# Optimization experiments

Hardware: AMD Instinct MI355X
Metric: run time of the kernel (lower is better)

Reference implementation:

```python
import jax, jax.numpy as jnp
import numpy as np

B, S, H = 2, 1024, 1024
NH, HD = 8, 128
E, TOPK, MI = 8, 2, 1024
SI = 2 * MI  # shared experts intermediate (n_shared_experts=2)
EPS = 1e-6
THETA = 10000.0


def setup_inputs() -> dict:
    key = jax.random.key(0)
    ks = jax.random.split(key, 16)
    w = lambda k, shp: (0.02 * jax.random.normal(k, shp, dtype=jnp.float32))
    # RoPE tables [S, HD]
    inv_freq = 1.0 / (THETA ** (np.arange(0, HD, 2, dtype=np.float32) / HD))
    t = np.arange(S, dtype=np.float32)
    freqs = np.outer(t, inv_freq)
    emb = np.concatenate([freqs, freqs], axis=-1)
    return {
        "hidden_states": jax.random.normal(ks[0], (B, S, H), dtype=jnp.float32),
        "ln1_w": jnp.ones((H,), jnp.float32),
        "ln2_w": jnp.ones((H,), jnp.float32),
        "q_w": w(ks[1], (H, H)),
        "k_w": w(ks[2], (H, H)),
        "v_w": w(ks[3], (H, H)),
        "o_w": w(ks[4], (H, H)),
        "cos": jnp.asarray(np.cos(emb), jnp.float32),
        "sin": jnp.asarray(np.sin(emb), jnp.float32),
        "gate_w": w(ks[5], (E, H)),
        "eg_w": w(ks[6], (E, MI, H)),
        "eu_w": w(ks[7], (E, MI, H)),
        "ed_w": w(ks[8], (E, H, MI)),
        "sg_w": w(ks[9], (SI, H)),
        "su_w": w(ks[10], (SI, H)),
        "sd_w": w(ks[11], (H, SI)),
    }


def _rmsnorm(x, w):
    return x * jax.lax.rsqrt(jnp.mean(x * x, axis=-1, keepdims=True) + EPS) * w


def _rotate_half(x):
    x1, x2 = jnp.split(x, 2, axis=-1)
    return jnp.concatenate([-x2, x1], axis=-1)


def _attention(x, q_w, k_w, v_w, o_w, cos, sin):
    b, s, h = x.shape
    q = (x @ q_w.T).reshape(b, s, NH, HD)
    k = (x @ k_w.T).reshape(b, s, NH, HD)
    v = (x @ v_w.T).reshape(b, s, NH, HD)
    c = cos[None, :s, None, :]
    sn = sin[None, :s, None, :]
    q = q * c + _rotate_half(q) * sn
    k = k * c + _rotate_half(k) * sn
    scores = jnp.einsum("bqhd,bkhd->bhqk", q, k) / jnp.sqrt(jnp.float32(HD))
    causal = jnp.tril(jnp.ones((s, s), dtype=bool))
    scores = jnp.where(causal[None, None], scores, -jnp.inf)
    p = jax.nn.softmax(scores, axis=-1)
    out = jnp.einsum("bhqk,bkhd->bqhd", p, v).reshape(b, s, h)
    return out @ o_w.T


def _mlp(x, gw, uw, dw):
    return (jax.nn.silu(x @ gw.T) * (x @ uw.T)) @ dw.T


def _moe(x, gate_w, eg_w, eu_w, ed_w, sg_w, su_w, sd_w):
    b, s, h = x.shape
    xt = x.reshape(-1, h)                              # [T, H]
    T = xt.shape[0]
    probs = jax.nn.softmax(xt @ gate_w.T, axis=-1)     # [T, E]
    rw, idx = jax.lax.top_k(probs, TOPK)               # [T, K]
    rw = rw / (jnp.sum(rw, axis=-1, keepdims=True) + 1e-20)  # norm_topk_prob
    # dense combine weights [T, E] (zero for unselected experts)
    w_full = jnp.zeros((T, E), xt.dtype).at[jnp.arange(T)[:, None], idx].add(rw)
    # dense all-expert compute, masked-combined (faithful to per-token loop math)
    g = jax.nn.silu(jnp.einsum("th,eih->tei", xt, eg_w))
    u = jnp.einsum("th,eih->tei", xt, eu_w)
    y = jnp.einsum("tei,ehi->teh", g * u, ed_w)        # [T, E, H]
    routed = jnp.einsum("teh,te->th", y, w_full)
    shared = _mlp(xt, sg_w, su_w, sd_w)
    return (routed + shared).reshape(b, s, h)


def reference(hidden_states, ln1_w, ln2_w, q_w, k_w, v_w, o_w, cos, sin,
              gate_w, eg_w, eu_w, ed_w, sg_w, su_w, sd_w):
    x = hidden_states
    x = x + _attention(_rmsnorm(x, ln1_w), q_w, k_w, v_w, o_w, cos, sin)
    x = x + _moe(_rmsnorm(x, ln2_w), gate_w, eg_w, eu_w, ed_w, sg_w, su_w, sd_w)
    return x
```

## Files before the change

### kernel.cpp

```cpp
#include <hip/hip_runtime.h>

#define B_   2
#define S_   1024
#define H_   1024
#define NH_  8
#define HD_  128
#define E_   8
#define MI_  1024
#define SI_  2048
#define T_   2048
#define CAP_ 2048

typedef unsigned short u16;
typedef __attribute__((ext_vector_type(4))) float f32x4;
typedef __attribute__((ext_vector_type(4))) unsigned short u16x4;
typedef __attribute__((ext_vector_type(8))) __bf16 bf16x8;

__device__ __forceinline__ u16 f2bf(float f) {
  unsigned int u = __builtin_bit_cast(unsigned int, f);
  u = (u + 0x7fffu + ((u >> 16) & 1u)) >> 16;
  return (u16)u;
}
__device__ __forceinline__ float bf2f(u16 u) {
  return __builtin_bit_cast(float, (unsigned int)u << 16);
}
__device__ __forceinline__ float wave_sum(float v) {
#pragma unroll
  for (int o = 32; o; o >>= 1) v += __shfl_down(v, o, 64);
  return v;
}
__device__ __forceinline__ void gll16(const u16* g, u16* l) {
  __builtin_amdgcn_global_load_lds((const __attribute__((address_space(1))) void*)g,
                                   (__attribute__((address_space(3))) void*)l, 16, 0, 0);
}

__global__ void cvt_all(const float* __restrict__ q_w, const float* __restrict__ k_w,
                        const float* __restrict__ v_w, const float* __restrict__ o_w,
                        const float* __restrict__ eg_w, const float* __restrict__ eu_w,
                        const float* __restrict__ ed_w, const float* __restrict__ sg_w,
                        const float* __restrict__ su_w, const float* __restrict__ sd_w,
                        u16* __restrict__ qwb, u16* __restrict__ egu, u16* __restrict__ edb,
                        u16* __restrict__ sgu, u16* __restrict__ sdb) {
  int bid = blockIdx.x, tid = threadIdx.x;
  const float* in;
  u16* outp;
  long f;
  if (bid < 4096) {
    f = ((long)bid * 256 + tid) * 4;
    int seg = (int)(f >> 20);
    in = (seg == 0) ? q_w : (seg == 1) ? k_w : (seg == 2) ? v_w : o_w;
    f32x4 v = *(const f32x4*)(in + (f & 1048575));
    u16x4 r;
#pragma unroll
    for (int c = 0; c < 4; c++) r[c] = f2bf(v[c]);
    *(u16x4*)(qwb + f) = r;
    return;
  } else if (bid < 20480) {
    int rel = bid - 4096;
    int zu = rel >= 8192;
    in = zu ? eu_w : eg_w;
    f = ((long)(rel & 8191) * 256 + tid) * 4;
    long e = f >> 20;
    long rem = f & 1048575;
    long i = rem >> 10, hh = rem & 1023;
    long orow = (i >> 4) * 32 + (i & 15) + (zu ? 16 : 0);
    outp = egu + (e * 2048 + orow) * 1024 + hh;
  } else if (bid < 28672) {
    f = ((long)(bid - 20480) * 256 + tid) * 4;
    in = ed_w;
    outp = edb + f;
  } else if (bid < 32768) {
    int rel = bid - 28672;
    int zu = rel >= 2048;
    in = zu ? su_w : sg_w;
    f = ((long)(rel & 2047) * 256 + tid) * 4;
    long i = f >> 10, hh = f & 1023;
    long orow = (i >> 4) * 32 + (i & 15) + (zu ? 16 : 0);
    outp = sgu + orow * 1024 + hh;
  } else {
    f = ((long)(bid - 32768) * 256 + tid) * 4;
    in = sd_w;
    outp = sdb + f;
  }
  f32x4 v = *(const f32x4*)(in + f);
  u16x4 r;
#pragma unroll
  for (int c = 0; c < 4; c++) r[c] = f2bf(v[c]);
  *(u16x4*)outp = r;
}

__global__ void rmsnorm_cvt(const float* __restrict__ x, const float* __restrict__ w,
                            u16* __restrict__ out) {
  int t = blockIdx.x, tid = threadIdx.x;
  f32x4 v = ((const f32x4*)(x + (long)t * H_))[tid];
  float ss = v[0]*v[0] + v[1]*v[1] + v[2]*v[2] + v[3]*v[3];
  __shared__ float red[4];
  float s = wave_sum(ss);
  if ((tid & 63) == 0) red[tid >> 6] = s;
  __syncthreads();
  float r = rsqrtf((red[0] + red[1] + red[2] + red[3]) * (1.0f / H_) + 1e-6f);
  f32x4 wv = ((const f32x4*)w)[tid];
  u16x4 o;
#pragma unroll
  for (int c = 0; c < 4; c++) o[c] = f2bf(v[c] * r * wv[c]);
  ((u16x4*)(out + (long)t * H_))[tid] = o;
}

__global__ void rmsnorm2_gate(const float* __restrict__ x1, const float* __restrict__ ln2w,
                              const float* __restrict__ gw, u16* __restrict__ xn,
                              int* __restrict__ eidx, float* __restrict__ aw) {
  int t = blockIdx.x, tid = threadIdx.x;
  int lane = tid & 63, wave = tid >> 6;
  f32x4 v = ((const f32x4*)(x1 + (long)t * H_))[tid];
  float ss = v[0]*v[0] + v[1]*v[1] + v[2]*v[2] + v[3]*v[3];
  __shared__ float redS[4];
  __shared__ float redE[4][E_];
  float s = wave_sum(ss);
  if (lane == 0) redS[wave] = s;
  __syncthreads();
  float r = rsqrtf((redS[0] + redS[1] + redS[2] + redS[3]) * (1.0f / H_) + 1e-6f);
  f32x4 wv = ((const f32x4*)ln2w)[tid];
  float xv[4];
  u16x4 o;
#pragma unroll
  for (int c = 0; c < 4; c++) { xv[c] = v[c] * r * wv[c]; o[c] = f2bf(xv[c]); }
  ((u16x4*)(xn + (long)t * H_))[tid] = o;
  float acc[E_];
#pragma unroll
  for (int e = 0; e < E_; e++) {
    f32x4 g = ((const f32x4*)(gw + (long)e * H_))[tid];
    acc[e] = xv[0]*g[0] + xv[1]*g[1] + xv[2]*g[2] + xv[3]*g[3];
  }
#pragma unroll
  for (int e = 0; e < E_; e++) acc[e] = wave_sum(acc[e]);
  if (lane == 0)
#pragma unroll
    for (int e = 0; e < E_; e++) redE[wave][e] = acc[e];
  __syncthreads();
  if (tid == 0) {
    float l[E_];
#pragma unroll
    for (int e = 0; e < E_; e++) l[e] = redE[0][e] + redE[1][e] + redE[2][e] + redE[3][e];
    float mx = l[0];
#pragma unroll
    for (int e = 1; e < E_; e++) mx = fmaxf(mx, l[e]);
    float p[E_], z = 0.f;
#pragma unroll
    for (int e = 0; e < E_; e++) { p[e] = __expf(l[e] - mx); z += p[e]; }
    int e0 = 0;
#pragma unroll
    for (int e = 1; e < E_; e++) if (p[e] > p[e0]) e0 = e;
    int e1 = (e0 == 0) ? 1 : 0;
#pragma unroll
    for (int e = 0; e < E_; e++) if (e != e0 && p[e] > p[e1]) e1 = e;
    float q0 = p[e0] / z, q1 = p[e1] / z;
    float invs = 1.0f / (q0 + q1 + 1e-20f);
    eidx[t * 2] = e0;
    eidx[t * 2 + 1] = e1;
    aw[t * 2] = q0 * invs;
    aw[t * 2 + 1] = q1 * invs;
  }
}

__global__ __launch_bounds__(256) void route_scan(const int* __restrict__ eidx,
                                                  int* __restrict__ arow,
                                                  int* __restrict__ cursor) {
  __shared__ int sc[E_][256];
  int tid = threadIdx.x;
  unsigned c0 = 0, c1 = 0;
  int ebuf[16];
#pragma unroll
  for (int i = 0; i < 16; i++) {
    int e = eidx[tid * 16 + i];
    ebuf[i] = e;
    if (e < 4) c0 += 1u << (8 * e); else c1 += 1u << (8 * (e - 4));
  }
#pragma unroll
  for (int e = 0; e < E_; e++)
    sc[e][tid] = (e < 4) ? (int)((c0 >> (8 * e)) & 0xff) : (int)((c1 >> (8 * (e - 4))) & 0xff);
  __syncthreads();
  for (int st = 1; st < 256; st <<= 1) {
    int v[E_];
#pragma unroll
    for (int e = 0; e < E_; e++) v[e] = (tid >= st) ? sc[e][tid - st] : 0;
    __syncthreads();
#pragma unroll
    for (int e = 0; e < E_; e++) sc[e][tid] += v[e];
    __syncthreads();
  }
  if (tid == 255)
#pragma unroll
    for (int e = 0; e < E_; e++) cursor[e] = sc[e][255];
  int base[E_];
#pragma unroll
  for (int e = 0; e < E_; e++) {
    int own = (e < 4) ? (int)((c0 >> (8 * e)) & 0xff) : (int)((c1 >> (8 * (e - 4))) & 0xff);
    base[e] = sc[e][tid] - own;
  }
  __syncthreads();
#pragma unroll
  for (int e = 0; e < E_; e++) sc[e][tid] = base[e];
  __syncthreads();
  unsigned r0 = 0, r1 = 0;
#pragma unroll
  for (int i = 0; i < 16; i++) {
    int e = ebuf[i];
    int run = (e < 4) ? (int)((r0 >> (8 * e)) & 0xff) : (int)((r1 >> (8 * (e - 4))) & 0xff);
    arow[tid * 16 + i] = e * CAP_ + sc[e][tid] + run;
    if (e < 4) r0 += 1u << (8 * e); else r1 += 1u << (8 * (e - 4));
  }
}

__global__ void rope_cvt(const float* __restrict__ qf, const float* __restrict__ cs,
                         const float* __restrict__ sn, u16* __restrict__ qbb) {
  const float* q = qf + (long)blockIdx.z * 2097152;
  u16* qb = qbb + (long)blockIdx.z * 2097152;
  int rid = blockIdx.x * 2 + (threadIdx.x >> 7);
  int d = threadIdx.x & 127;
  int h = rid & (NH_ - 1);
  int bs = rid >> 3;
  int s = bs & (S_ - 1);
  int b = bs >> 10;
  long base = (long)rid * HD_;
  float v = q[base + d];
  float o = (d < 64) ? (-q[base + d + 64]) : q[base + d - 64];
  float res = v * cs[s * HD_ + d] + o * sn[s * HD_ + d];
  qb[((long)((b * NH_ + h) * S_ + s)) * HD_ + d] = f2bf(res);
}

__global__ void vtrans(const float* __restrict__ v, u16* __restrict__ vt) {
  int bh = blockIdx.z, b = bh >> 3, h = bh & 7;
  int s0 = blockIdx.x * 32, d0 = blockIdx.y * 32;
  __shared__ u16 tile[32][33];
  for (int i = threadIdx.y; i < 32; i += 8) {
    float val = v[(((long)(b * S_ + s0 + i)) * NH_ + h) * HD_ + d0 + threadIdx.x];
    tile[i][threadIdx.x] = f2bf(val);
  }
  __syncthreads();
  for (int i = threadIdx.y; i < 32; i += 8) {
    vt[((long)bh * HD_ + d0 + i) * S_ + s0 + threadIdx.x] = tile[threadIdx.x][i];
  }
}

__global__ __launch_bounds__(256) void flash_part(
    const u16* __restrict__ qb, const u16* __restrict__ kb,
    const u16* __restrict__ vt, u16* __restrict__ Po,
    float* __restrict__ Pm, float* __restrict__ Pl) {
  int item = blockIdx.x;
  int bh = blockIdx.y;
  int qt, ch;
  if (item < 4)       { qt = item;                    ch = 0; }
  else if (item < 12) { qt = 4 + ((item - 4) >> 1);   ch = (item - 4) & 1; }
  else if (item < 24) { qt = 8 + (item - 12) / 3;     ch = (item - 12) % 3; }
  else                { qt = 12 + ((item - 24) >> 2); ch = (item - 24) & 3; }
  int j0 = ch * 4, j1 = min(j0 + 4, qt + 1);

  int tid = threadIdx.x;
  int wavei = tid >> 6, lane = tid & 63;
  int la = lane & 15, qd = lane >> 4;

  __shared__ __align__(16) u16 Ks[64 * 128];
  __shared__ __align__(16) u16 Vs[128 * 64];
  __shared__ __align__(16) u16 Ps[4][16 * 64];

  bf16x8 qf[4];
  const u16* qrow = qb + ((long)bh * S_ + qt * 64 + wavei * 16 + la) * HD_;
#pragma unroll
  for (int ks = 0; ks < 4; ks++)
    qf[ks] = *(const bf16x8*)(qrow + ks * 32 + qd * 8);

  f32x4 oacc[8];
#pragma unroll
  for (int nf = 0; nf < 8; nf++) oacc[nf] = (f32x4){0.f, 0.f, 0.f, 0.f};
  float m_i[4], l_i[4];
#pragma unroll
  for (int r = 0; r < 4; r++) { m_i[r] = -1e30f; l_i[r] = 0.f; }

  const u16* Kbase = kb + (long)bh * S_ * HD_;
  const u16* Vbase = vt + (long)bh * HD_ * S_;
  const float scale = 0.08838834764831845f;
  u16* pw = (u16*)Ps[wavei];
  int swz = la & 7;

  for (int j = j0; j < j1; j++) {
    __syncthreads();
#pragma unroll
    for (int t = 0; t < 4; t++) {
      int blk = t * 4 + wavei;
      int kr = blk * 4 + (lane >> 4);
      int kc = (lane & 15) ^ (kr & 7);
      gll16(Kbase + ((long)j * 64 + kr) * 128 + kc * 8, Ks + blk * 512);
      int vr = blk * 8 + (lane >> 3);
      int vc = (lane & 7) ^ (vr & 7);
      gll16(Vbase + (long)vr * 1024 + j * 64 + vc * 8, Vs + blk * 512);
    }
    __syncthreads();

    f32x4 sacc[4];
#pragma unroll
    for (int jf = 0; jf < 4; jf++) sacc[jf] = (f32x4){0.f, 0.f, 0.f, 0.f};
#pragma unroll
    for (int ks = 0; ks < 4; ks++)
#pragma unroll
      for (int jf = 0; jf < 4; jf++) {
        bf16x8 kfrag = *(const bf16x8*)(Ks + (jf * 16 + la) * 128 + ((ks * 4 + qd) ^ swz) * 8);
        sacc[jf] = __builtin_amdgcn_mfma_f32_16x16x32_bf16(qf[ks], kfrag, sacc[jf], 0, 0, 0);
      }

    float sv[4][4];
    int qglob = qt * 64 + wavei * 16 + qd * 4;
#pragma unroll
    for (int jf = 0; jf < 4; jf++) {
      int kglob = j * 64 + jf * 16 + la;
#pragma unroll
      for (int r = 0; r < 4; r++)
        sv[jf][r] = (kglob <= qglob + r) ? sacc[jf][r] * scale : -1e30f;
    }
    float mnew[4], alpha[4];
#pragma unroll
    for (int r = 0; r < 4; r++) {
      float mx = fmaxf(fmaxf(sv[0][r], sv[1][r]), fmaxf(sv[2][r], sv[3][r]));
#pragma unroll
      for (int o = 1; o < 16; o <<= 1) mx = fmaxf(mx, __shfl_xor(mx, o, 64));
      mnew[r] = fmaxf(m_i[r], mx);
      alpha[r] = __expf(m_i[r] - mnew[r]);
      m_i[r] = mnew[r];
    }
#pragma unroll
    for (int r = 0; r < 4; r++) {
      float sum = 0.f;
#pragma unroll
      for (int jf = 0; jf < 4; jf++) {
        float p = __expf(sv[jf][r] - mnew[r]);
        sv[jf][r] = p;
        sum += p;
      }
#pragma unroll
      for (int o = 1; o < 16; o <<= 1) sum += __shfl_xor(sum, o, 64);
      l_i[r] = l_i[r] * alpha[r] + sum;
    }
#pragma unroll
    for (int jf = 0; jf < 4; jf++)
#pragma unroll
      for (int r = 0; r < 4; r++) {
        int rp = qd * 4 + r;
        int e = jf * 16 + la;
        pw[rp * 64 + (((e >> 3) ^ (rp & 7)) << 3) + (e & 7)] = f2bf(sv[jf][r]);
      }
#pragma unroll
    for (int nf = 0; nf < 8; nf++)
#pragma unroll
      for (int r = 0; r < 4; r++) oacc[nf][r] *= alpha[r];
#pragma unroll
    for (int ks = 0; ks < 2; ks++) {
      bf16x8 pfrag = *(const bf16x8*)(pw + la * 64 + ((ks * 4 + qd) ^ swz) * 8);
#pragma unroll
      for (int nf = 0; nf < 8; nf++) {
        bf16x8 vfrag = *(const bf16x8*)(Vs + (nf * 16 + la) * 64 + (((ks * 4 + qd) & 7) ^ swz) * 8);
        oacc[nf] = __builtin_amdgcn_mfma_f32_16x16x32_bf16(pfrag, vfrag, oacc[nf], 0, 0, 0);
      }
    }
  }

  int pidx = (bh * 16 + qt) * 4 + ch;
  int rowb = wavei * 16 + qd * 4;
  u16* pob = Po + ((long)pidx * 64 + rowb) * 128;
#pragma unroll
  for (int r = 0; r < 4; r++)
#pragma unroll
    for (int nf = 0; nf < 8; nf++)
      pob[(long)r * 128 + nf * 16 + la] = f2bf(oacc[nf][r]);
  if (la == 0)
#pragma unroll
    for (int r = 0; r < 4; r++) {
      Pm[pidx * 64 + rowb + r] = m_i[r];
      Pl[pidx * 64 + rowb + r] = l_i[r];
    }
}

__global__ __launch_bounds__(256) void attn_merge(
    const u16* __restrict__ Po, const float* __restrict__ Pm,
    const float* __restrict__ Pl, u16* __restrict__ attn) {
  int qt = blockIdx.x, bh = blockIdx.y;
  int b = bh >> 3, h = bh & 7;
  int nch = (qt >> 2) + 1;
  int t = threadIdx.x;
  int row = t >> 2, cg = (t & 3) * 32;
  long base = (long)(bh * 16 + qt) * 4;
  float mv[4], wv[4];
  float M = -1e30f;
  for (int c = 0; c < nch; c++) { mv[c] = Pm[(base + c) * 64 + row]; M = fmaxf(M, mv[c]); }
  float L = 0.f;
  for (int c = 0; c < nch; c++) { wv[c] = __expf(mv[c] - M); L += wv[c] * Pl[(base + c) * 64 + row]; }
  float inv = 1.0f / L;
  f32x4 o[8];
#pragma unroll
  for (int k = 0; k < 8; k++) o[k] = (f32x4){0.f, 0.f, 0.f, 0.f};
  for (int c = 0; c < nch; c++) {
    const u16x4* src = (const u16x4*)(Po + ((base + c) * 64 + row) * 128 + cg);
#pragma unroll
    for (int k = 0; k < 8; k++) {
      u16x4 sv = src[k];
#pragma unroll
      for (int e = 0; e < 4; e++) o[k][e] += bf2f(sv[e]) * wv[c];
    }
  }
  u16* dst = attn + ((long)b * S_ + qt * 64 + row) * H_ + h * HD_ + cg;
#pragma unroll
  for (int k = 0; k < 8; k++) {
    u16x4 ov;
#pragma unroll
    for (int c = 0; c < 4; c++) ov[c] = f2bf(o[k][c] * inv);
    ((u16x4*)dst)[k] = ov;
  }
}

__global__ void gather_rows(const u16* __restrict__ xn, const int* __restrict__ arow,
                            u16* __restrict__ xg) {
  int a = blockIdx.x;
  int t = a >> 1;
  int row = arow[a];
  u16x4 v = ((const u16x4*)(xn + (long)t * H_))[threadIdx.x];
  ((u16x4*)(xg + (long)row * H_))[threadIdx.x] = v;
}

__global__ void final_combine(const float* __restrict__ x1, const float* __restrict__ ys,
                              const u16* __restrict__ y, const int* __restrict__ arow,
                              const float* __restrict__ aw, float* __restrict__ out) {
  int t = blockIdx.x;
  int i = threadIdx.x * 4;
  int r0 = arow[t * 2], r1 = arow[t * 2 + 1];
  float w0 = aw[t * 2], w1 = aw[t * 2 + 1];
  f32x4 a = *(const f32x4*)(x1 + (long)t * H_ + i);
  f32x4 b = *(const f32x4*)(ys + (long)t * H_ + i);
  u16x4 y0 = *(const u16x4*)(y + (long)r0 * H_ + i);
  u16x4 y1 = *(const u16x4*)(y + (long)r1 * H_ + i);
  f32x4 o;
#pragma unroll
  for (int c = 0; c < 4; c++)
    o[c] = a[c] + b[c] + w0 * bf2f(y0[c]) + w1 * bf2f(y1[c]);
  *(f32x4*)(out + (long)t * H_ + i) = o;
}

template <int MT, int STORE_BF16, int ADD_RES, int FUSE_SILU>
__global__ __launch_bounds__(256) void gemm_bt(
    const u16* __restrict__ Ag, const u16* __restrict__ Bg, void* __restrict__ Cg,
    const float* __restrict__ Res, int K, int lda, int ldb, int ldc,
    long sAz, long sBz, long sCz, const int* __restrict__ mlimit) {
  constexpr int MR = MT / 32;
  int z = blockIdx.z;
  int m0 = blockIdx.y * MT, n0 = blockIdx.x * 128;
  if (mlimit && m0 >= mlimit[z]) return;
  const u16* A = Ag + z * sAz;
  const u16* B = Bg + z * sBz;
  long cbase = (long)z * sCz;

  __shared__ __align__(16) u16 As[MT * 64];
  __shared__ __align__(16) u16 Bs[128 * 64];
  int tid = threadIdx.x;
  int lane = tid & 63, wave = tid >> 6;
  int wm = (wave & 1) * (MT / 2), wn = (wave >> 1) * 64;
  int la = lane & 15, qd = lane >> 4;
  int sr = lane >> 3;
  int scs = (lane & 7) ^ (sr & 7);

  const u16* ap[MT / 32];
  const u16* bp[4];
#pragma unroll
  for (int t = 0; t < MT / 32; t++)
    ap[t] = A + (long)(m0 + t * 32 + wave * 8 + sr) * lda + scs * 8;
#pragma unroll
  for (int t = 0; t < 4; t++)
    bp[t] = B + (long)(n0 + t * 32 + wave * 8 + sr) * ldb + scs * 8;

  f32x4 acc[MR][4];
#pragma unroll
  for (int i = 0; i < MR; i++)
#pragma unroll
    for (int j = 0; j < 4; j++) acc[i][j] = (f32x4){0.f, 0.f, 0.f, 0.f};

  int sw = la & 7;
  for (int k0 = 0; k0 < K; k0 += 64) {
    __syncthreads();
#pragma unroll
    for (int t = 0; t < MT / 32; t++)
      gll16(ap[t] + k0, As + (t * 32 + wave * 8) * 64);
#pragma unroll
    for (int t = 0; t < 4; t++)
      gll16(bp[t] + k0, Bs + (t * 32 + wave * 8) * 64);
    __syncthreads();
#pragma unroll
    for (int kk = 0; kk < 2; kk++) {
      bf16x8 af[MR], bf[4];
#pragma unroll
      for (int i = 0; i < MR; i++)
        af[i] = *(const bf16x8*)(As + (wm + i * 16 + la) * 64 + (((kk * 4 + qd) ^ sw) << 3));
#pragma unroll
      for (int j = 0; j < 4; j++)
        bf[j] = *(const bf16x8*)(Bs + (wn + j * 16 + la) * 64 + (((kk * 4 + qd) ^ sw) << 3));
#pragma unroll
      for (int i = 0; i < MR; i++)
#pragma unroll
        for (int j = 0; j < 4; j++)
          acc[i][j] = __builtin_amdgcn_mfma_f32_16x16x32_bf16(af[i], bf[j], acc[i][j], 0, 0, 0);
    }
  }

  if (FUSE_SILU) {
#pragma unroll
    for (int i = 0; i < MR; i++) {
#pragma unroll
      for (int jp = 0; jp < 2; jp++) {
        int hcol = ((n0 + wn) >> 1) + (jp << 4) + la;
#pragma unroll
        for (int r = 0; r < 4; r++) {
          int row = m0 + wm + i * 16 + qd * 4 + r;
          float g = acc[i][jp * 2][r], u = acc[i][jp * 2 + 1][r];
          float sg = g / (1.f + __expf(-g));
          ((u16*)Cg)[cbase + (long)row * ldc + hcol] = f2bf(sg * u);
        }
      }
    }
  } else {
#pragma unroll
    for (int i = 0; i < MR; i++) {
#pragma unroll
      for (int j = 0; j < 4; j++) {
        int col = n0 + wn + j * 16 + la;
#pragma unroll
        for (int r = 0; r < 4; r++) {
          int row = m0 + wm + i * 16 + qd * 4 + r;
          float v = acc[i][j][r];
          long ci = cbase + (long)row * ldc + col;
          if (ADD_RES) v += Res[(long)row * ldc + col];
          if (STORE_BF16) ((u16*)Cg)[ci] = f2bf(v);
          else ((float*)Cg)[ci] = v;
        }
      }
    }
  }
}

extern "C" void kernel_launch(void* const* d_in, const int* in_sizes, int n_in,
                              void* d_out, int out_size, void* d_ws, size_t ws_size,
                              hipStream_t stream) {
  const float* hidden = (const float*)d_in[0];
  const float* ln1w = (const float*)d_in[1];
  const float* ln2w = (const float*)d_in[2];
  const float* q_w = (const float*)d_in[3];
  const float* k_w = (const float*)d_in[4];
  const float* v_w = (const float*)d_in[5];
  const float* o_w = (const float*)d_in[6];
  const float* cosp = (const float*)d_in[7];
  const float* sinp = (const float*)d_in[8];
  const float* gate_w = (const float*)d_in[9];
  const float* eg_w = (const float*)d_in[10];
  const float* eu_w = (const float*)d_in[11];
  const float* ed_w = (const float*)d_in[12];
  const float* sg_w = (const float*)d_in[13];
  const float* su_w = (const float*)d_in[14];
  const float* sd_w = (const float*)d_in[15];
  float* out = (float*)d_out;

  char* w = (char*)d_ws;
  const size_t MB = 1u << 20;
  u16* qwb = (u16*)(w + 0 * MB);
  u16* egu = (u16*)(w + 8 * MB);
  u16* edb = (u16*)(w + 40 * MB);
  u16* sgu = (u16*)(w + 56 * MB);
  u16* sdb = (u16*)(w + 64 * MB);
  float* x1 = (float*)(w + 68 * MB);
  u16* xn = (u16*)(w + 76 * MB);
  u16* attn = (u16*)(w + 80 * MB);
  int* cursor = (int*)(w + 84 * MB);
  int* arow = (int*)(w + 84 * MB + 1024);
  float* aw = (float*)(w + 84 * MB + 20 * 1024);
  int* eidx = (int*)(w + 84 * MB + 40 * 1024);
  float* qf = (float*)(w + 85 * MB);
  float* kf = (float*)(w + 93 * MB);
  float* vf = (float*)(w + 101 * MB);
  u16* qb = (u16*)(w + 109 * MB);
  u16* kb = (u16*)(w + 113 * MB);
  u16* vt = (u16*)(w + 117 * MB);
  u16* Po = (u16*)(w + 121 * MB);
  float* Pm = (float*)(w + 155 * MB);
  float* Pl = (float*)(w + 156 * MB);
  u16* xg = (u16*)(w + 85 * MB);
  u16* hbuf = (u16*)(w + 121 * MB);
  u16* y = (u16*)(w + 157 * MB);
  u16* hs = (u16*)(w + 189 * MB);
  float* ys = (float*)(w + 197 * MB);

  const long M1 = 1048576, M2 = 2097152;

  cvt_all<<<34816, 256, 0, stream>>>(q_w, k_w, v_w, o_w, eg_w, eu_w, ed_w,
                                     sg_w, su_w, sd_w, qwb, egu, edb, sgu, sdb);

  rmsnorm_cvt<<<T_, 256, 0, stream>>>(hidden, ln1w, xn);
  gemm_bt<128, 0, 0, 0><<<dim3(8, 16, 3), 256, 0, stream>>>(
      xn, qwb, qf, nullptr, 1024, 1024, 1024, 1024, 0, M1, M2, nullptr);
  rope_cvt<<<dim3(8192, 1, 2), 256, 0, stream>>>(qf, cosp, sinp, qb);
  vtrans<<<dim3(32, 4, 16), dim3(32, 8), 0, stream>>>(vf, vt);
  flash_part<<<dim3(40, 16), 256, 0, stream>>>(qb, kb, vt, Po, Pm, Pl);
  attn_merge<<<dim3(16, 16), 256, 0, stream>>>(Po, Pm, Pl, attn);
  gemm_bt<64, 0, 1, 0><<<dim3(8, 32, 1), 256, 0, stream>>>(
      attn, qwb + 3 * M1, x1, hidden, 1024, 1024, 1024, 1024, 0, 0, 0, nullptr);

  rmsnorm2_gate<<<T_, 256, 0, stream>>>(x1, ln2w, gate_w, xn, eidx, aw);
  route_scan<<<1, 256, 0, stream>>>(eidx, arow, cursor);
  gather_rows<<<4096, 256, 0, stream>>>(xn, arow, xg);
  gemm_bt<128, 1, 0, 1><<<dim3(16, 16, 8), 256, 0, stream>>>(
      xg, egu, hbuf, nullptr, 1024, 1024, 1024, MI_,
      (long)CAP_ * H_, (long)2 * MI_ * H_, (long)CAP_ * MI_, cursor);
  gemm_bt<128, 1, 0, 0><<<dim3(8, 16, 8), 256, 0, stream>>>(
      hbuf, edb, y, nullptr, 1024, 1024, 1024, 1024,
      (long)CAP_ * MI_, (long)H_ * MI_, (long)CAP_ * H_, cursor);
  gemm_bt<128, 1, 0, 1><<<dim3(32, 16, 1), 256, 0, stream>>>(
      xn, sgu, hs, nullptr, 1024, 1024, 1024, SI_, 0, 0, 0, nullptr);
  gemm_bt<64, 0, 0, 0><<<dim3(8, 32, 1), 256, 0, stream>>>(
      hs, sdb, ys, nullptr, 2048, 2048, 2048, 1024, 0, 0, 0, nullptr);

  final_combine<<<T_, 256, 0, stream>>>(x1, ys, y, arow, aw, out);
}
```

Measured before the change: 427.4 us.

## Widen weight conversion, store QKV in bf16, and fuse MoE gather into GEMM

The weight conversion kernel now has each thread handle 16 elements with 8-wide bf16 stores, which cuts the block count by a factor of four. The QKV GEMM writes bf16 instead of fp32, so rope and the V transpose read half the bytes. The MoE gather kernel is removed: route_scan writes a row-to-token index table and the expert up/gate GEMM loads A rows indirectly through it, so the gathered copy is never materialised. This costs a memset and an extra index load per A row, and rounding Q/K to bf16 before RoPE adds a little precision loss.

```diff
diff --git a/kernel.cpp b/kernel.cpp
--- a/kernel.cpp
+++ b/kernel.cpp
@@ -14,6 +14,7 @@
 typedef unsigned short u16;
 typedef __attribute__((ext_vector_type(4))) float f32x4;
 typedef __attribute__((ext_vector_type(4))) unsigned short u16x4;
+typedef __attribute__((ext_vector_type(8))) unsigned short u16x8;
 typedef __attribute__((ext_vector_type(8))) __bf16 bf16x8;
 
 __device__ __forceinline__ u16 f2bf(float f) {
@@ -42,51 +43,53 @@
                         u16* __restrict__ qwb, u16* __restrict__ egu, u16* __restrict__ edb,
                         u16* __restrict__ sgu, u16* __restrict__ sdb) {
   int bid = blockIdx.x, tid = threadIdx.x;
-  const float* in;
-  u16* outp;
-  long f;
-  if (bid < 4096) {
-    f = ((long)bid * 256 + tid) * 4;
+  const float* src;
+  u16* dst;
+  if (bid < 1024) {
+    long f = (long)bid * 4096 + tid * 16;
     int seg = (int)(f >> 20);
-    in = (seg == 0) ? q_w : (seg == 1) ? k_w : (seg == 2) ? v_w : o_w;
-    f32x4 v = *(const f32x4*)(in + (f & 1048575));
-    u16x4 r;
-#pragma unroll
-    for (int c = 0; c < 4; c++) r[c] = f2bf(v[c]);
-    *(u16x4*)(qwb + f) = r;
-    return;
-  } else if (bid < 20480) {
-    int rel = bid - 4096;
-    int zu = rel >= 8192;
-    in = zu ? eu_w : eg_w;
-    f = ((long)(rel & 8191) * 256 + tid) * 4;
-    long e = f >> 20;
-    long rem = f & 1048575;
+    const float* in = (seg == 0) ? q_w : (seg == 1) ? k_w : (seg == 2) ? v_w : o_w;
+    src = in + (f & 1048575);
+    dst = qwb + f;
+  } else if (bid < 5120) {
+    int rel = bid - 1024;
+    int zu = rel >= 2048;
+    long fl = (long)(rel & 2047) * 4096 + tid * 16;
+    long e = fl >> 20;
+    long rem = fl & 1048575;
     long i = rem >> 10, hh = rem & 1023;
     long orow = (i >> 4) * 32 + (i & 15) + (zu ? 16 : 0);
-    outp = egu + (e * 2048 + orow) * 1024 + hh;
-  } else if (bid < 28672) {
-    f = ((long)(bid - 20480) * 256 + tid) * 4;
-    in = ed_w;
-    outp = edb + f;
-  } else if (bid < 32768) {
-    int rel = bid - 28672;
-    int zu = rel >= 2048;
-    in = zu ? su_w : sg_w;
-    f = ((long)(rel & 2047) * 256 + tid) * 4;
-    long i = f >> 10, hh = f & 1023;
+    src = (zu ? eu_w : eg_w) + fl;
+    dst = egu + (e * 2048 + orow) * 1024 + hh;
+  } else if (bid < 7168) {
+    long fl = (long)(bid - 5120) * 4096 + tid * 16;
+    src = ed_w + fl;
+    dst = edb + fl;
+  } else if (bid < 8192) {
+    int rel = bid - 7168;
+    int zu = rel >= 512;
+    long fl = (long)(rel & 511) * 4096 + tid * 16;
+    long i = fl >> 10, hh = fl & 1023;
     long orow = (i >> 4) * 32 + (i & 15) + (zu ? 16 : 0);
-    outp = sgu + orow * 1024 + hh;
+    src = (zu ? su_w : sg_w) + fl;
+    dst = sgu + orow * 1024 + hh;
   } else {
-    f = ((long)(bid - 32768) * 256 + tid) * 4;
-    in = sd_w;
-    outp = sdb + f;
-  }
-  f32x4 v = *(const f32x4*)(in + f);
-  u16x4 r;
-#pragma unroll
-  for (int c = 0; c < 4; c++) r[c] = f2bf(v[c]);
-  *(u16x4*)outp = r;
+    long fl = (long)(bid - 8192) * 4096 + tid * 16;
+    src = sd_w + fl;
+    dst = sdb + fl;
+  }
+  f32x4 v0 = ((const f32x4*)src)[0];
+  f32x4 v1 = ((const f32x4*)src)[1];
+  f32x4 v2 = ((const f32x4*)src)[2];
+  f32x4 v3 = ((const f32x4*)src)[3];
+  u16x8 r0, r1;
+#pragma unroll
+  for (int c = 0; c < 4; c++) {
+    r0[c] = f2bf(v0[c]); r0[c + 4] = f2bf(v1[c]);
+    r1[c] = f2bf(v2[c]); r1[c + 4] = f2bf(v3[c]);
+  }
+  ((u16x8*)dst)[0] = r0;
+  ((u16x8*)dst)[1] = r1;
 }
 
 __global__ void rmsnorm_cvt(const float* __restrict__ x, const float* __restrict__ w,
@@ -164,7 +167,8 @@
 
 __global__ __launch_bounds__(256) void route_scan(const int* __restrict__ eidx,
                                                   int* __restrict__ arow,
-                                                  int* __restrict__ cursor) {
+                                                  int* __restrict__ cursor,
+                                                  int* __restrict__ itok) {
   __shared__ int sc[E_][256];
   int tid = threadIdx.x;
   unsigned c0 = 0, c1 = 0;
@@ -206,14 +210,16 @@
   for (int i = 0; i < 16; i++) {
     int e = ebuf[i];
     int run = (e < 4) ? (int)((r0 >> (8 * e)) & 0xff) : (int)((r1 >> (8 * (e - 4))) & 0xff);
-    arow[tid * 16 + i] = e * CAP_ + sc[e][tid] + run;
+    int row = e * CAP_ + sc[e][tid] + run;
+    arow[tid * 16 + i] = row;
+    itok[row] = (tid * 16 + i) >> 1;
     if (e < 4) r0 += 1u << (8 * e); else r1 += 1u << (8 * (e - 4));
   }
 }
 
-__global__ void rope_cvt(const float* __restrict__ qf, const float* __restrict__ cs,
+__global__ void rope_cvt(const u16* __restrict__ qf, const float* __restrict__ cs,
                          const float* __restrict__ sn, u16* __restrict__ qbb) {
-  const float* q = qf + (long)blockIdx.z * 2097152;
+  const u16* q = qf + (long)blockIdx.z * 2097152;
   u16* qb = qbb + (long)blockIdx.z * 2097152;
   int rid = blockIdx.x * 2 + (threadIdx.x >> 7);
   int d = threadIdx.x & 127;
@@ -222,19 +228,18 @@
   int s = bs & (S_ - 1);
   int b = bs >> 10;
   long base = (long)rid * HD_;
-  float v = q[base + d];
-  float o = (d < 64) ? (-q[base + d + 64]) : q[base + d - 64];
+  float v = bf2f(q[base + d]);
+  float o = (d < 64) ? (-bf2f(q[base + d + 64])) : bf2f(q[base + d - 64]);
   float res = v * cs[s * HD_ + d] + o * sn[s * HD_ + d];
   qb[((long)((b * NH_ + h) * S_ + s)) * HD_ + d] = f2bf(res);
 }
 
-__global__ void vtrans(const float* __restrict__ v, u16* __restrict__ vt) {
+__global__ void vtrans(const u16* __restrict__ v, u16* __restrict__ vt) {
   int bh = blockIdx.z, b = bh >> 3, h = bh & 7;
   int s0 = blockIdx.x * 32, d0 = blockIdx.y * 32;
   __shared__ u16 tile[32][33];
   for (int i = threadIdx.y; i < 32; i += 8) {
-    float val = v[(((long)(b * S_ + s0 + i)) * NH_ + h) * HD_ + d0 + threadIdx.x];
-    tile[i][threadIdx.x] = f2bf(val);
+    tile[i][threadIdx.x] = v[(((long)(b * S_ + s0 + i)) * NH_ + h) * HD_ + d0 + threadIdx.x];
   }
   __syncthreads();
   for (int i = threadIdx.y; i < 32; i += 8) {
@@ -415,15 +420,6 @@
   }
 }
 
-__global__ void gather_rows(const u16* __restrict__ xn, const int* __restrict__ arow,
-                            u16* __restrict__ xg) {
-  int a = blockIdx.x;
-  int t = a >> 1;
-  int row = arow[a];
-  u16x4 v = ((const u16x4*)(xn + (long)t * H_))[threadIdx.x];
-  ((u16x4*)(xg + (long)row * H_))[threadIdx.x] = v;
-}
-
 __global__ void final_combine(const float* __restrict__ x1, const float* __restrict__ ys,
                               const u16* __restrict__ y, const int* __restrict__ arow,
                               const float* __restrict__ aw, float* __restrict__ out) {
@@ -442,16 +438,17 @@
   *(f32x4*)(out + (long)t * H_ + i) = o;
 }
 
-template <int MT, int STORE_BF16, int ADD_RES, int FUSE_SILU>
+template <int MT, int STORE_BF16, int ADD_RES, int FUSE_SILU, int IND>
 __global__ __launch_bounds__(256) void gemm_bt(
     const u16* __restrict__ Ag, const u16* __restrict__ Bg, void* __restrict__ Cg,
     const float* __restrict__ Res, int K, int lda, int ldb, int ldc,
-    long sAz, long sBz, long sCz, const int* __restrict__ mlimit) {
+    long sAz, long sBz, long sCz, const int* __restrict__ mlimit,
+    const int* __restrict__ itok) {
   constexpr int MR = MT / 32;
   int z = blockIdx.z;
   int m0 = blockIdx.y * MT, n0 = blockIdx.x * 128;
   if (mlimit && m0 >= mlimit[z]) return;
-  const u16* A = Ag + z * sAz;
+  const u16* A = Ag + (IND ? 0 : z * sAz);
   const u16* B = Bg + z * sBz;
   long cbase = (long)z * sCz;
 
@@ -467,8 +464,11 @@
   const u16* ap[MT / 32];
   const u16* bp[4];
 #pragma unroll
-  for (int t = 0; t < MT / 32; t++)
-    ap[t] = A + (long)(m0 + t * 32 + wave * 8 + sr) * lda + scs * 8;
+  for (int t = 0; t < MT / 32; t++) {
+    int rloc = m0 + t * 32 + wave * 8 + sr;
+    long arow_g = IND ? (long)itok[(long)z * CAP_ + rloc] : (long)rloc;
+    ap[t] = A + arow_g * lda + scs * 8;
+  }
 #pragma unroll
   for (int t = 0; t < 4; t++)
     bp[t] = B + (long)(n0 + t * 32 + wave * 8 + sr) * ldb + scs * 8;
@@ -576,16 +576,14 @@
   int* arow = (int*)(w + 84 * MB + 1024);
   float* aw = (float*)(w + 84 * MB + 20 * 1024);
   int* eidx = (int*)(w + 84 * MB + 40 * 1024);
-  float* qf = (float*)(w + 85 * MB);
-  float* kf = (float*)(w + 93 * MB);
-  float* vf = (float*)(w + 101 * MB);
+  int* itok = (int*)(w + 84 * MB + 60 * 1024);
+  u16* qkvb = (u16*)(w + 85 * MB);
   u16* qb = (u16*)(w + 109 * MB);
   u16* kb = (u16*)(w + 113 * MB);
   u16* vt = (u16*)(w + 117 * MB);
   u16* Po = (u16*)(w + 121 * MB);
   float* Pm = (float*)(w + 155 * MB);
   float* Pl = (float*)(w + 156 * MB);
-  u16* xg = (u16*)(w + 85 * MB);
   u16* hbuf = (u16*)(w + 121 * MB);
   u16* y = (u16*)(w + 157 * MB);
   u16* hs = (u16*)(w + 189 * MB);
@@ -593,32 +591,32 @@
 
   const long M1 = 1048576, M2 = 2097152;
 
-  cvt_all<<<34816, 256, 0, stream>>>(q_w, k_w, v_w, o_w, eg_w, eu_w, ed_w,
-                                     sg_w, su_w, sd_w, qwb, egu, edb, sgu, sdb);
+  cvt_all<<<8704, 256, 0, stream>>>(q_w, k_w, v_w, o_w, eg_w, eu_w, ed_w,
+                                    sg_w, su_w, sd_w, qwb, egu, edb, sgu, sdb);
 
   rmsnorm_cvt<<<T_, 256, 0, stream>>>(hidden, ln1w, xn);
-  gemm_bt<128, 0, 0, 0><<<dim3(8, 16, 3), 256, 0, stream>>>(
-      xn, qwb, qf, nullptr, 1024, 1024, 1024, 1024, 0, M1, M2, nullptr);
-  rope_cvt<<<dim3(8192, 1, 2), 256, 0, stream>>>(qf, cosp, sinp, qb);
-  vtrans<<<dim3(32, 4, 16), dim3(32, 8), 0, stream>>>(vf, vt);
+  gemm_bt<128, 1, 0, 0, 0><<<dim3(8, 16, 3), 256, 0, stream>>>(
+      xn, qwb, qkvb, nullptr, 1024, 1024, 1024, 1024, 0, M1, M2, nullptr, nullptr);
+  rope_cvt<<<dim3(8192, 1, 2), 256, 0, stream>>>(qkvb, cosp, sinp, qb);
+  vtrans<<<dim3(32, 4, 16), dim3(32, 8), 0, stream>>>(qkvb + 2 * M2, vt);
   flash_part<<<dim3(40, 16), 256, 0, stream>>>(qb, kb, vt, Po, Pm, Pl);
   attn_merge<<<dim3(16, 16), 256, 0, stream>>>(Po, Pm, Pl, attn);
-  gemm_bt<64, 0, 1, 0><<<dim3(8, 32, 1), 256, 0, stream>>>(
-      attn, qwb + 3 * M1, x1, hidden, 1024, 1024, 1024, 1024, 0, 0, 0, nullptr);
+  gemm_bt<64, 0, 1, 0, 0><<<dim3(8, 32, 1), 256, 0, stream>>>(
+      attn, qwb + 3 * M1, x1, hidden, 1024, 1024, 1024, 1024, 0, 0, 0, nullptr, nullptr);
 
   rmsnorm2_gate<<<T_, 256, 0, stream>>>(x1, ln2w, gate_w, xn, eidx, aw);
-  route_scan<<<1, 256, 0, stream>>>(eidx, arow, cursor);
-  gather_rows<<<4096, 256, 0, stream>>>(xn, arow, xg);
-  gemm_bt<128, 1, 0, 1><<<dim3(16, 16, 8), 256, 0, stream>>>(
-      xg, egu, hbuf, nullptr, 1024, 1024, 1024, MI_,
-      (long)CAP_ * H_, (long)2 * MI_ * H_, (long)CAP_ * MI_, cursor);
-  gemm_bt<128, 1, 0, 0><<<dim3(8, 16, 8), 256, 0, stream>>>(
+  hipMemsetAsync(itok, 0, E_ * CAP_ * 4, stream);
+  route_scan<<<1, 256, 0, stream>>>(eidx, arow, cursor, itok);
+  gemm_bt<128, 1, 0, 1, 1><<<dim3(16, 16, 8), 256, 0, stream>>>(
+      xn, egu, hbuf, nullptr, 1024, 1024, 1024, MI_,
+      0, (long)2 * MI_ * H_, (long)CAP_ * MI_, cursor, itok);
+  gemm_bt<128, 1, 0, 0, 0><<<dim3(8, 16, 8), 256, 0, stream>>>(
       hbuf, edb, y, nullptr, 1024, 1024, 1024, 1024,
-      (long)CAP_ * MI_, (long)H_ * MI_, (long)CAP_ * H_, cursor);
-  gemm_bt<128, 1, 0, 1><<<dim3(32, 16, 1), 256, 0, stream>>>(
-      xn, sgu, hs, nullptr, 1024, 1024, 1024, SI_, 0, 0, 0, nullptr);
-  gemm_bt<64, 0, 0, 0><<<dim3(8, 32, 1), 256, 0, stream>>>(
-      hs, sdb, ys, nullptr, 2048, 2048, 2048, 1024, 0, 0, 0, nullptr);
+      (long)CAP_ * MI_, (long)H_ * MI_, (long)CAP_ * H_, cursor, nullptr);
+  gemm_bt<128, 1, 0, 1, 0><<<dim3(32, 16, 1), 256, 0, stream>>>(
+      xn, sgu, hs, nullptr, 1024, 1024, 1024, SI_, 0, 0, 0, nullptr, nullptr);
+  gemm_bt<64, 0, 0, 0, 0><<<dim3(8, 32, 1), 256, 0, stream>>>(
+      hs, sdb, ys, nullptr, 2048, 2048, 2048, 1024, 0, 0, 0, nullptr, nullptr);
 
   final_combine<<<T_, 256, 0, stream>>>(x1, ys, y, arow, aw, out);
 }
```

After: 422.5 us. About the same (-1.2%).
